# Performance work log

Measured on AMD Instinct MI355X. Metric: run time of the kernel, lower is better.

The kernel has to match this reference:

```python
import jax, jax.numpy as jnp
import numpy as np

N = 100000      # nodes
E = 1600000     # directed edges (avg degree 16)
F_IN = 128      # n_features
D = 128         # embed_dim
OUT = 1         # out_features


def setup_inputs() -> dict:
    key = jax.random.key(0)
    ks = jax.random.split(key, 8)
    x = jax.random.normal(ks[0], (N, F_IN), dtype=jnp.float32)
    edge_index = jax.random.randint(ks[1], (2, E), 0, N, dtype=jnp.int64)
    # GCNConv weights (glorot-ish scale) and biases
    W1 = jax.random.normal(ks[2], (F_IN, D), dtype=jnp.float32) * (1.0 / np.sqrt(F_IN))
    b1 = jnp.zeros((D,), dtype=jnp.float32)
    W2 = jax.random.normal(ks[3], (D, D), dtype=jnp.float32) * (1.0 / np.sqrt(D))
    b2 = jnp.zeros((D,), dtype=jnp.float32)
    Wfc = jax.random.normal(ks[4], (D, OUT), dtype=jnp.float32) * (1.0 / np.sqrt(D))
    bfc = jnp.zeros((OUT,), dtype=jnp.float32)
    return {"x": x, "edge_index": edge_index, "W1": W1, "b1": b1,
            "W2": W2, "b2": b2, "Wfc": Wfc, "bfc": bfc}


def _gcn_conv(x, src, dst, W, b, n):
    """PyG GCNConv: h = X W; symmetric normalization with self-loops; scatter-add; + b."""
    h = x @ W                                  # [n, d] transform first
    loops = jnp.arange(n, dtype=src.dtype)
    s = jnp.concatenate([src, loops])          # self-loops appended
    d = jnp.concatenate([dst, loops])
    deg = jax.ops.segment_sum(jnp.ones_like(d, dtype=h.dtype), d, num_segments=n)
    dinv = jnp.where(deg > 0, jax.lax.rsqrt(deg), 0.0)
    norm = dinv[s] * dinv[d]                   # [E+n]
    msg = h[s] * norm[:, None]                 # gather + scale
    out = jax.ops.segment_sum(msg, d, num_segments=n)  # scatter-add to targets
    return out + b


def reference(x, edge_index, W1, b1, W2, b2, Wfc, bfc):
    src, dst = edge_index[0], edge_index[1]
    n = x.shape[0]
    h = jnp.tanh(_gcn_conv(x, src, dst, W1, b1, n))
    # F.dropout with training=False -> identity (eval mode)
    embeddings = jnp.tanh(_gcn_conv(h, src, dst, W2, b2, n))
    out = jax.nn.sigmoid(embeddings @ Wfc + bfc)
    return (out, embeddings)
```

## Files before the change

kernel.cpp:

```cpp
#include <hip/hip_runtime.h>
#include <math.h>

#define CAP 64
#define NR 16
#define EPB 4096
#define PCAP 112640

typedef unsigned int uint;
typedef unsigned short ushort;
typedef __attribute__((ext_vector_type(8))) short bf16x8;
typedef __attribute__((ext_vector_type(4))) float f32x4;

__device__ __forceinline__ ushort f2bf(float f) {
  union { float f; uint u; } v; v.f = f;
  uint u = v.u;
  return (ushort)((u + 0x7fffu + ((u >> 16) & 1u)) >> 16);
}
__device__ __forceinline__ float bflo(uint p) {
  union { uint u; float f; } v; v.u = p << 16; return v.f;
}
__device__ __forceinline__ float bfhi(uint p) {
  union { uint u; float f; } v; v.u = p & 0xffff0000u; return v.f;
}
__device__ __forceinline__ uint pk2(float a, float b) {
  return (uint)f2bf(a) | ((uint)f2bf(b) << 16);
}
__device__ __forceinline__ uint pk2r(float a, float b, float& ra, float& rb) {
  ushort ha = f2bf(a), hb = f2bf(b);
  union { uint u; float f; } va, vb;
  va.u = (uint)ha << 16; vb.u = (uint)hb << 16;
  ra = a - va.f; rb = b - vb.f;
  return (uint)ha | ((uint)hb << 16);
}
__device__ __forceinline__ int drange(int d) {
  return (int)(((unsigned long long)(uint)d * 687195ull) >> 32);
}


__global__ __launch_bounds__(256) void k_partition(const int* __restrict__ src,
    const int* __restrict__ dst, int* __restrict__ cur,
    int2* __restrict__ part, int E) {
  __shared__ int lcnt[NR * 256];
  __shared__ int basev[NR];
  const int t = threadIdx.x;
  const int b0 = blockIdx.x * EPB;
  #pragma unroll
  for (int r = 0; r < NR; ++r) lcnt[r * 256 + t] = 0;
  __syncthreads();
  int es[16], ed[16];
  #pragma unroll
  for (int j = 0; j < 16; ++j) {
    int e = b0 + j * 256 + t;
    int d = (e < E) ? dst[e] : -1;
    es[j] = (e < E) ? src[e] : 0;
    ed[j] = d;
    if (d >= 0) lcnt[drange(d) * 256 + t]++;
  }
  __syncthreads();
  if (t < NR) {
    int run = 0;
    #pragma unroll 8
    for (int k = 0; k < 256; ++k) { int v = lcnt[t * 256 + k]; lcnt[t * 256 + k] = run; run += v; }
    basev[t] = atomicAdd(cur + t, run);
  }
  __syncthreads();
  #pragma unroll
  for (int j = 0; j < 16; ++j) {
    int d = ed[j];
    if (d >= 0) {
      int r = drange(d);
      int off = basev[r] + lcnt[r * 256 + t]++;
      if (off < PCAP) part[(size_t)r * PCAP + off] = make_int2(es[j], d);
    }
  }
}


__global__ __launch_bounds__(256) void k_bucket2(const int2* __restrict__ part,
    const int* __restrict__ cur, int* __restrict__ cnt, int* __restrict__ bucket) {
  const int t = threadIdx.x;
  const int xcd = blockIdx.x & 7;
  const int slot = blockIdx.x >> 3;
  const int S = (gridDim.x >> 3) * 256;
  for (int rr = xcd; rr < NR; rr += 8) {
    int cE = min(cur[rr], PCAP);
    const int2* p = part + (size_t)rr * PCAP;
    int e = slot * 256 + t;
    for (; e + 3 * S < cE; e += 4 * S) {
      int2 p0 = p[e], p1 = p[e + S], p2 = p[e + 2 * S], p3 = p[e + 3 * S];
      int k0 = atomicAdd(cnt + p0.y, 1);
      int k1 = atomicAdd(cnt + p1.y, 1);
      int k2 = atomicAdd(cnt + p2.y, 1);
      int k3 = atomicAdd(cnt + p3.y, 1);
      if (k0 < CAP) bucket[(size_t)p0.y * CAP + k0] = p0.x;
      if (k1 < CAP) bucket[(size_t)p1.y * CAP + k1] = p1.x;
      if (k2 < CAP) bucket[(size_t)p2.y * CAP + k2] = p2.x;
      if (k3 < CAP) bucket[(size_t)p3.y * CAP + k3] = p3.x;
    }
    for (; e < cE; e += S) {
      int2 pe = p[e];
      int k = atomicAdd(cnt + pe.y, 1);
      if (k < CAP) bucket[(size_t)pe.y * CAP + k] = pe.x;
    }
  }
}

__global__ __launch_bounds__(256) void k_dinv(const int* __restrict__ cnt,
    float* __restrict__ dinv, int n, const float* __restrict__ W2,
    uint* __restrict__ Wp) {
  int i = blockIdx.x * 256 + threadIdx.x;
  if (i < n) dinv[i] = rsqrtf((float)cnt[i] + 1.0f);
  if (i < 64 * 128) {
    int k2 = i >> 7, col = i & 127;
    Wp[i] = pk2(W2[k2 * 256 + col], W2[k2 * 256 + 128 + col]);
  }
}


__global__ __launch_bounds__(256) void k_gemm_mfma(const float* __restrict__ X,
    const float* __restrict__ W, const float* __restrict__ dinv,
    ushort* __restrict__ H, int n, int ntiles) {
  const int lane = threadIdx.x & 63;
  const int quad = lane >> 4;
  const int sub  = lane & 15;
  const int wid    = (blockIdx.x * 256 + threadIdx.x) >> 6;
  const int nwaves = (gridDim.x * 256) >> 6;

  union { bf16x8 v; uint u[4]; } Bh[4][8];
  #pragma unroll
  for (int ki = 0; ki < 4; ++ki) {
    #pragma unroll
    for (int ct = 0; ct < 8; ++ct) {
      const float* wp = W + (ki * 32 + quad * 8) * 128 + ct * 16 + sub;
      Bh[ki][ct].u[0] = pk2(wp[0],   wp[128]);
      Bh[ki][ct].u[1] = pk2(wp[256], wp[384]);
      Bh[ki][ct].u[2] = pk2(wp[512], wp[640]);
      Bh[ki][ct].u[3] = pk2(wp[768], wp[896]);
    }
  }

  for (int tile = wid; tile < ntiles; tile += nwaves) {
    int base = tile * 16;
    int row  = base + sub;
    if (row >= n) row = n - 1;
    const float* xp = X + (size_t)row * 128 + quad * 8;

    f32x4 acc[8];
    #pragma unroll
    for (int ct = 0; ct < 8; ++ct) acc[ct] = (f32x4){0.f, 0.f, 0.f, 0.f};

    #pragma unroll
    for (int ki = 0; ki < 4; ++ki) {
      float4 xa = *(const float4*)(xp + ki * 32);
      float4 xb = *(const float4*)(xp + ki * 32 + 4);
      union { bf16x8 v; uint u[4]; } ah, al;
      float r0,r1,r2,r3,r4,r5,r6,r7;
      ah.u[0] = pk2r(xa.x, xa.y, r0, r1);
      ah.u[1] = pk2r(xa.z, xa.w, r2, r3);
      ah.u[2] = pk2r(xb.x, xb.y, r4, r5);
      ah.u[3] = pk2r(xb.z, xb.w, r6, r7);
      al.u[0] = pk2(r0, r1);
      al.u[1] = pk2(r2, r3);
      al.u[2] = pk2(r4, r5);
      al.u[3] = pk2(r6, r7);
      #pragma unroll
      for (int ct = 0; ct < 8; ++ct) {
        acc[ct] = __builtin_amdgcn_mfma_f32_16x16x32_bf16(ah.v, Bh[ki][ct].v, acc[ct], 0, 0, 0);
        acc[ct] = __builtin_amdgcn_mfma_f32_16x16x32_bf16(al.v, Bh[ki][ct].v, acc[ct], 0, 0, 0);
      }
    }

    float dv[4];
    #pragma unroll
    for (int r = 0; r < 4; ++r) {
      int rr = base + quad * 4 + r;
      dv[r] = (rr < n) ? dinv[rr] : 0.f;
    }
    #pragma unroll
    for (int ct = 0; ct < 8; ++ct) {
      #pragma unroll
      for (int r = 0; r < 4; ++r) {
        int rr = base + quad * 4 + r;
        if (rr < n)
          H[(size_t)rr * 128 + ct * 16 + sub] = f2bf(acc[ct][r] * dv[r]);
      }
    }
  }
}


__device__ __forceinline__ void acc8(float* a, uint4 v, bool act) {
  if (act) {
    a[0] += bflo(v.x); a[1] += bfhi(v.x); a[2] += bflo(v.y); a[3] += bfhi(v.y);
    a[4] += bflo(v.z); a[5] += bfhi(v.z); a[6] += bflo(v.w); a[7] += bfhi(v.w);
  }
}

__device__ __forceinline__ void gather8(const uint4* __restrict__ H4,
    const int* __restrict__ bk, int nc, int c, int cmax, int sub, float* a) {
  int i = 0;
  for (; i + 8 <= cmax; i += 8) {
    int4 sA = *(const int4*)(bk + i);
    int4 sB = *(const int4*)(bk + i + 4);
    int s0 = (i     < c) ? sA.x : nc;
    int s1 = (i + 1 < c) ? sA.y : nc;
    int s2 = (i + 2 < c) ? sA.z : nc;
    int s3 = (i + 3 < c) ? sA.w : nc;
    int s4 = (i + 4 < c) ? sB.x : nc;
    int s5 = (i + 5 < c) ? sB.y : nc;
    int s6 = (i + 6 < c) ? sB.z : nc;
    int s7 = (i + 7 < c) ? sB.w : nc;
    uint4 v0 = H4[(size_t)s0 * 16 + sub];
    uint4 v1 = H4[(size_t)s1 * 16 + sub];
    uint4 v2 = H4[(size_t)s2 * 16 + sub];
    uint4 v3 = H4[(size_t)s3 * 16 + sub];
    uint4 v4 = H4[(size_t)s4 * 16 + sub];
    uint4 v5 = H4[(size_t)s5 * 16 + sub];
    uint4 v6 = H4[(size_t)s6 * 16 + sub];
    uint4 v7 = H4[(size_t)s7 * 16 + sub];
    acc8(a, v0, i     < c); acc8(a, v1, i + 1 < c);
    acc8(a, v2, i + 2 < c); acc8(a, v3, i + 3 < c);
    acc8(a, v4, i + 4 < c); acc8(a, v5, i + 5 < c);
    acc8(a, v6, i + 6 < c); acc8(a, v7, i + 7 < c);
  }
  if (i + 4 <= cmax) {
    int4 sA = *(const int4*)(bk + i);
    int s0 = (i     < c) ? sA.x : nc;
    int s1 = (i + 1 < c) ? sA.y : nc;
    int s2 = (i + 2 < c) ? sA.z : nc;
    int s3 = (i + 3 < c) ? sA.w : nc;
    uint4 v0 = H4[(size_t)s0 * 16 + sub];
    uint4 v1 = H4[(size_t)s1 * 16 + sub];
    uint4 v2 = H4[(size_t)s2 * 16 + sub];
    uint4 v3 = H4[(size_t)s3 * 16 + sub];
    acc8(a, v0, i < c); acc8(a, v1, i + 1 < c);
    acc8(a, v2, i + 2 < c); acc8(a, v3, i + 3 < c);
    i += 4;
  }
  for (; i < cmax; ++i) {
    int s = (i < c) ? bk[i] : nc;
    uint4 v0 = H4[(size_t)s * 16 + sub];
    acc8(a, v0, i < c);
  }
}


template <bool FC>
__global__ __launch_bounds__(256, 6) void k_agg4(const ushort* __restrict__ H,
    const int* __restrict__ cnt, const int* __restrict__ bucket,
    const float* __restrict__ dinv, const float* __restrict__ bias,
    const float* __restrict__ Wfc, const float* __restrict__ bfc,
    float* __restrict__ OUT, float* __restrict__ OUTV, int n) {
  const int wave = (blockIdx.x * 256 + threadIdx.x) >> 6;
  const int lane = threadIdx.x & 63;
  const int sub = lane & 15;
  const int node = wave * 4 + (lane >> 4);
  const bool an = node < n;
  const int nc = an ? node : 0;
  const uint4* H4 = (const uint4*)H;

  uint4 v = H4[(size_t)nc * 16 + sub];
  float a[8] = {bflo(v.x),bfhi(v.x),bflo(v.y),bfhi(v.y),
                bflo(v.z),bfhi(v.z),bflo(v.w),bfhi(v.w)};
  int c = an ? min(cnt[nc], CAP) : 0;
  int cmax = max(c, __shfl_xor(c, 16)); cmax = max(cmax, __shfl_xor(cmax, 32));
  gather8(H4, bucket + (size_t)nc * CAP, nc, c, cmax, sub, a);

  float dn = an ? dinv[nc] : 0.f;
  float4 b0 = ((const float4*)bias)[sub * 2];
  float4 b1 = ((const float4*)bias)[sub * 2 + 1];
  float o[8];
  o[0] = tanhf(a[0]*dn + b0.x); o[1] = tanhf(a[1]*dn + b0.y);
  o[2] = tanhf(a[2]*dn + b0.z); o[3] = tanhf(a[3]*dn + b0.w);
  o[4] = tanhf(a[4]*dn + b1.x); o[5] = tanhf(a[5]*dn + b1.y);
  o[6] = tanhf(a[6]*dn + b1.z); o[7] = tanhf(a[7]*dn + b1.w);
  if (an) {
    float4* dst0 = (float4*)(OUT + (size_t)node * 128 + sub * 8);
    dst0[0] = make_float4(o[0], o[1], o[2], o[3]);
    dst0[1] = make_float4(o[4], o[5], o[6], o[7]);
  }
  if (FC) {
    float4 w0 = ((const float4*)Wfc)[sub * 2];
    float4 w1 = ((const float4*)Wfc)[sub * 2 + 1];
    float p = o[0]*w0.x + o[1]*w0.y + o[2]*w0.z + o[3]*w0.w
            + o[4]*w1.x + o[5]*w1.y + o[6]*w1.z + o[7]*w1.w;
    p += __shfl_down(p, 8, 16);
    p += __shfl_down(p, 4, 16);
    p += __shfl_down(p, 2, 16);
    p += __shfl_down(p, 1, 16);
    if (an && sub == 0) OUTV[node] = 1.0f / (1.0f + expf(-(p + bfc[0])));
  }
}


__global__ __launch_bounds__(256, 6) void k_agg_gemm(const ushort* __restrict__ H,
    const int* __restrict__ cnt, const int* __restrict__ bucket,
    const float* __restrict__ dinv, const float* __restrict__ bias,
    const uint* __restrict__ Wp, ushort* __restrict__ H2, int n) {
  __shared__ uint4 Lhi[16][17];
  __shared__ uint4 Llo[16][17];
  const int wid  = threadIdx.x >> 6;
  const int lane = threadIdx.x & 63;
  const int quad = lane >> 4, sub = lane & 15;
  const int trow = wid * 4 + quad;
  const int node = blockIdx.x * 16 + trow;
  const bool an = node < n;
  const int nc = an ? node : 0;
  const uint4* H4 = (const uint4*)H;

  uint4 v = H4[(size_t)nc * 16 + sub];
  float a[8] = {bflo(v.x),bfhi(v.x),bflo(v.y),bfhi(v.y),
                bflo(v.z),bfhi(v.z),bflo(v.w),bfhi(v.w)};
  int c = an ? min(cnt[nc], CAP) : 0;
  int cmax = max(c, __shfl_xor(c, 16)); cmax = max(cmax, __shfl_xor(cmax, 32));
  gather8(H4, bucket + (size_t)nc * CAP, nc, c, cmax, sub, a);

  float dn = an ? dinv[nc] : 0.f;
  float4 b0 = ((const float4*)bias)[sub * 2];
  float4 b1 = ((const float4*)bias)[sub * 2 + 1];
  float o0 = tanhf(a[0]*dn + b0.x), o1 = tanhf(a[1]*dn + b0.y);
  float o2 = tanhf(a[2]*dn + b0.z), o3 = tanhf(a[3]*dn + b0.w);
  float o4 = tanhf(a[4]*dn + b1.x), o5 = tanhf(a[5]*dn + b1.y);
  float o6 = tanhf(a[6]*dn + b1.z), o7 = tanhf(a[7]*dn + b1.w);

  union { uint u[4]; uint4 q; } ah, al;
  float r0,r1,r2,r3,r4,r5,r6,r7;
  ah.u[0] = pk2r(o0, o1, r0, r1);
  ah.u[1] = pk2r(o2, o3, r2, r3);
  ah.u[2] = pk2r(o4, o5, r4, r5);
  ah.u[3] = pk2r(o6, o7, r6, r7);
  al.u[0] = pk2(r0, r1);
  al.u[1] = pk2(r2, r3);
  al.u[2] = pk2(r4, r5);
  al.u[3] = pk2(r6, r7);
  Lhi[trow][sub] = ah.q;
  Llo[trow][sub] = al.q;
  __syncthreads();

  const int ct0 = wid * 2;
  union { bf16x8 v; uint u[4]; } B0[4], B1[4];
  #pragma unroll
  for (int ki = 0; ki < 4; ++ki) {
    #pragma unroll
    for (int j = 0; j < 4; ++j) {
      int krow = (ki * 16 + quad * 4 + j) * 128;
      B0[ki].u[j] = Wp[krow + ct0 * 16 + sub];
      B1[ki].u[j] = Wp[krow + (ct0 + 1) * 16 + sub];
    }
  }
  f32x4 acc0 = (f32x4){0.f,0.f,0.f,0.f};
  f32x4 acc1 = (f32x4){0.f,0.f,0.f,0.f};
  #pragma unroll
  for (int ki = 0; ki < 4; ++ki) {
    union { uint4 q; bf16x8 v; } Ah, Al;
    Ah.q = Lhi[sub][ki * 4 + quad];
    Al.q = Llo[sub][ki * 4 + quad];
    acc0 = __builtin_amdgcn_mfma_f32_16x16x32_bf16(Ah.v, B0[ki].v, acc0, 0, 0, 0);
    acc0 = __builtin_amdgcn_mfma_f32_16x16x32_bf16(Al.v, B0[ki].v, acc0, 0, 0, 0);
    acc1 = __builtin_amdgcn_mfma_f32_16x16x32_bf16(Ah.v, B1[ki].v, acc1, 0, 0, 0);
    acc1 = __builtin_amdgcn_mfma_f32_16x16x32_bf16(Al.v, B1[ki].v, acc1, 0, 0, 0);
  }
  const int base16 = blockIdx.x * 16;
  #pragma unroll
  for (int r = 0; r < 4; ++r) {
    int rr = base16 + quad * 4 + r;
    if (rr < n) {
      float dv = dinv[rr];
      H2[(size_t)rr * 128 + ct0 * 16 + sub]       = f2bf(acc0[r] * dv);
      H2[(size_t)rr * 128 + (ct0 + 1) * 16 + sub] = f2bf(acc1[r] * dv);
    }
  }
}


extern "C" void kernel_launch(void* const* d_in, const int* in_sizes, int n_in,
                              void* d_out, int out_size, void* d_ws, size_t ws_size,
                              hipStream_t stream) {
  const float* x   = (const float*)d_in[0];
  const int*   ei  = (const int*)d_in[1];
  const float* W1  = (const float*)d_in[2];
  const float* b1  = (const float*)d_in[3];
  const float* W2  = (const float*)d_in[4];
  const float* b2  = (const float*)d_in[5];
  const float* Wfc = (const float*)d_in[6];
  const float* bfc = (const float*)d_in[7];

  const int N = in_sizes[0] / 128;
  const int E = in_sizes[1] / 2;
  const int* src = ei;
  const int* dst = ei + E;

  float* out = (float*)d_out;
  float* emb = out + N;

  char* ws = (char*)d_ws;
  size_t used = 0;
  auto take = [&](size_t bytes) {
    char* p = ws + used; used += (bytes + 255) & ~(size_t)255; return p;
  };
  int*    cnt    = (int*)   take((size_t)N * 4);
  float*  dinv   = (float*) take((size_t)N * 4);
  int*    cur    = (int*)   take(64 * 4);
  uint*   Wp     = (uint*)  take(64 * 128 * 4);
  int*    bucket = (int*)   take((size_t)N * CAP * 4);
  ushort* bufH   = (ushort*)take((size_t)N * 128 * 2);
  size_t h2bytes = (((size_t)N * 128 * 2) + 255) & ~(size_t)255;
  bool fused = (used + h2bytes) <= ws_size;
  ushort* bufH2 = fused ? (ushort*)take((size_t)N * 128 * 2) : nullptr;
  int2*   part  = (int2*)bufH;

  const int ntiles = (N + 15) / 16;
  const int aggBlocks = (N + 15) / 16;

  hipMemsetAsync(cnt, 0, (size_t)N * 4, stream);
  hipMemsetAsync(cur, 0, 64 * 4, stream);

  k_partition<<<(E + EPB - 1) / EPB, 256, 0, stream>>>(src, dst, cur, part, E);
  k_bucket2<<<2048, 256, 0, stream>>>(part, cur, cnt, bucket);
  k_dinv<<<(N + 255) / 256, 256, 0, stream>>>(cnt, dinv, N, W2, Wp);

  k_gemm_mfma<<<512, 256, 0, stream>>>(x, W1, dinv, bufH, N, ntiles);

  if (fused) {
    k_agg_gemm<<<aggBlocks, 256, 0, stream>>>(bufH, cnt, bucket, dinv, b1, Wp, bufH2, N);
    k_agg4<true><<<aggBlocks, 256, 0, stream>>>(bufH2, cnt, bucket, dinv, b2,
                                                Wfc, bfc, emb, out, N);
  } else {
    k_agg4<false><<<aggBlocks, 256, 0, stream>>>(bufH, cnt, bucket, dinv, b1,
                                                 nullptr, nullptr, emb, nullptr, N);
    k_gemm_mfma<<<512, 256, 0, stream>>>(emb, W2, dinv, bufH, N, ntiles);
    k_agg4<true><<<aggBlocks, 256, 0, stream>>>(bufH, cnt, bucket, dinv, b2,
                                                Wfc, bfc, emb, out, N);
  }
}
```

Measured before the change: 372.2 us.

## Bucket edges per range with LDS counters and fold dinv computation in

Replaces the global-atomic bucketing kernel and the separate dinv kernel with a single kernel that uses one 1024-thread block per destination range. Each block counts in-degree with shared-memory atomics, writes buckets, then writes cnt and dinv, which also removes the cnt memset and one launch. The cost is that only 16 blocks run, each streaming about 100k edges, so most of the GPU sits idle during this stage.

```diff
diff --git a/kernel.cpp b/kernel.cpp
--- a/kernel.cpp
+++ b/kernel.cpp
@@ -5,6 +5,7 @@
 #define NR 16
 #define EPB 4096
 #define PCAP 112640
+#define RNG 6250
 
 typedef unsigned int uint;
 typedef unsigned short ushort;
@@ -76,43 +77,35 @@
 }
 
 
-__global__ __launch_bounds__(256) void k_bucket2(const int2* __restrict__ part,
-    const int* __restrict__ cur, int* __restrict__ cnt, int* __restrict__ bucket) {
+__global__ __launch_bounds__(1024) void k_sortbkt(const int2* __restrict__ part,
+    const int* __restrict__ cur, int* __restrict__ cnt, int* __restrict__ bucket,
+    float* __restrict__ dinv, const float* __restrict__ W2, uint* __restrict__ Wp, int n) {
+  __shared__ int lc[RNG];
+  const int r = blockIdx.x;
   const int t = threadIdx.x;
-  const int xcd = blockIdx.x & 7;
-  const int slot = blockIdx.x >> 3;
-  const int S = (gridDim.x >> 3) * 256;
-  for (int rr = xcd; rr < NR; rr += 8) {
-    int cE = min(cur[rr], PCAP);
-    const int2* p = part + (size_t)rr * PCAP;
-    int e = slot * 256 + t;
-    for (; e + 3 * S < cE; e += 4 * S) {
-      int2 p0 = p[e], p1 = p[e + S], p2 = p[e + 2 * S], p3 = p[e + 3 * S];
-      int k0 = atomicAdd(cnt + p0.y, 1);
-      int k1 = atomicAdd(cnt + p1.y, 1);
-      int k2 = atomicAdd(cnt + p2.y, 1);
-      int k3 = atomicAdd(cnt + p3.y, 1);
-      if (k0 < CAP) bucket[(size_t)p0.y * CAP + k0] = p0.x;
-      if (k1 < CAP) bucket[(size_t)p1.y * CAP + k1] = p1.x;
-      if (k2 < CAP) bucket[(size_t)p2.y * CAP + k2] = p2.x;
-      if (k3 < CAP) bucket[(size_t)p3.y * CAP + k3] = p3.x;
-    }
-    for (; e < cE; e += S) {
-      int2 pe = p[e];
-      int k = atomicAdd(cnt + pe.y, 1);
-      if (k < CAP) bucket[(size_t)pe.y * CAP + k] = pe.x;
-    }
-  }
-}
-
-__global__ __launch_bounds__(256) void k_dinv(const int* __restrict__ cnt,
-    float* __restrict__ dinv, int n, const float* __restrict__ W2,
-    uint* __restrict__ Wp) {
-  int i = blockIdx.x * 256 + threadIdx.x;
-  if (i < n) dinv[i] = rsqrtf((float)cnt[i] + 1.0f);
-  if (i < 64 * 128) {
-    int k2 = i >> 7, col = i & 127;
-    Wp[i] = pk2(W2[k2 * 256 + col], W2[k2 * 256 + 128 + col]);
+  for (int i = t; i < RNG; i += 1024) lc[i] = 0;
+  for (int i = t; i < 512; i += 1024) {
+    int idx = r * 512 + i;
+    int k2 = idx >> 7, col = idx & 127;
+    Wp[idx] = pk2(W2[k2 * 256 + col], W2[k2 * 256 + 128 + col]);
+  }
+  __syncthreads();
+  const int base = r * RNG;
+  const int cE = min(cur[r], PCAP);
+  const int2* p = part + (size_t)r * PCAP;
+  for (int e = t; e < cE; e += 1024) {
+    int2 pe = p[e];
+    int k = atomicAdd(&lc[pe.y - base], 1);
+    if (k < CAP) bucket[(size_t)pe.y * CAP + k] = pe.x;
+  }
+  __syncthreads();
+  for (int i = t; i < RNG; i += 1024) {
+    int node = base + i;
+    if (node < n) {
+      int c = lc[i];
+      cnt[node] = c;
+      dinv[node] = rsqrtf((float)c + 1.0f);
+    }
   }
 }
 
@@ -412,12 +405,10 @@
   const int ntiles = (N + 15) / 16;
   const int aggBlocks = (N + 15) / 16;
 
-  hipMemsetAsync(cnt, 0, (size_t)N * 4, stream);
   hipMemsetAsync(cur, 0, 64 * 4, stream);
 
   k_partition<<<(E + EPB - 1) / EPB, 256, 0, stream>>>(src, dst, cur, part, E);
-  k_bucket2<<<2048, 256, 0, stream>>>(part, cur, cnt, bucket);
-  k_dinv<<<(N + 255) / 256, 256, 0, stream>>>(cnt, dinv, N, W2, Wp);
+  k_sortbkt<<<NR, 1024, 0, stream>>>(part, cur, cnt, bucket, dinv, W2, Wp, N);
 
   k_gemm_mfma<<<512, 256, 0, stream>>>(x, W1, dinv, bufH, N, ntiles);
 
```

After: 404.7 us. 8.7% more time.
